# Performance work log

Hardware: AMD Instinct MI355X
Metric: run time of the kernel (lower is better)

The kernel has to match this reference:

```python
import jax, jax.numpy as jnp
import numpy as np

B, S, P, D = 256, 2048, 64, 80

def setup_inputs() -> dict:
    key = jax.random.key(0)
    k1, k2, k3, k4 = jax.random.split(key, 4)
    enc_out = jax.random.normal(k1, (B, S, D), dtype=jnp.float32)
    dec_out = jax.random.normal(k2, (B, P, D), dtype=jnp.float32)
    attn_mask = jax.random.randint(k3, (B, S), 0, 2) > 0  # True = masked
    # guarantee at least one unmasked position per row (avoid NaN softmax)
    attn_mask = attn_mask.at[:, 0].set(False)
    W = jax.random.normal(k4, (D, D), dtype=jnp.float32) * (1.0 / np.sqrt(D))
    return {"enc_out": enc_out, "dec_out": dec_out, "attn_mask": attn_mask, "W": W}

def reference(enc_out, dec_out, attn_mask, W):
    # query = Linear(dec_out) with no bias: y = x @ W^T
    query = jnp.einsum('bpd,ed->bpe', dec_out, W)          # (B, P, D)
    # unscaled attention scores (no 1/sqrt(d) in original)
    weight = jnp.einsum('bpd,bsd->bps', query, enc_out)    # (B, P, S)
    neg = jnp.finfo(weight.dtype).min
    weight = jnp.where(attn_mask[:, None, :], neg, weight)
    weight = jax.nn.softmax(weight, axis=-1)
    context = jnp.einsum('bps,bsd->bpd', weight, enc_out)  # (B, P, D)
    return context
```

## Files before the change

### kernel.cpp

```cpp
#include <hip/hip_runtime.h>

#define NB 256
#define NS 2048
#define NP 64
#define ND 80
#define STILE 128
#define NTILE 16
#define NTHREADS 1024
#define LOG2E 1.4426950408889634f

typedef __attribute__((ext_vector_type(4))) float f32x4;
typedef __attribute__((ext_vector_type(2))) __fp16 fp16x2;
typedef __attribute__((ext_vector_type(8))) _Float16 f16x8;
typedef __attribute__((ext_vector_type(4))) unsigned short u16x4;
typedef unsigned short u16;

#define SMEM_BYTES 60944

__device__ __forceinline__ float E2(float x) { return __builtin_amdgcn_exp2f(x); }
__device__ __forceinline__ unsigned pkh(float lo, float hi) {
  union { fp16x2 h; unsigned u; } cv;
  cv.h = __builtin_amdgcn_cvt_pkrtz(lo, hi);
  return cv.u;
}

__device__ __forceinline__ f32x4 mfma16f(f16x8 a, f16x8 b, f32x4 c) {
  return __builtin_amdgcn_mfma_f32_16x16x32_f16(a, b, c, 0, 0, 0);
}

__global__ __launch_bounds__(NTHREADS, 4)
void DecoderAttention_62989990363717_kernel(const float* __restrict__ enc,
                                            const float* __restrict__ dec,
                                            const int* __restrict__ maskp,
                                            const float* __restrict__ W,
                                            float* __restrict__ out)
{
  __shared__ __align__(16) char smem[SMEM_BYTES];

  u16* ehP    = (u16*)smem;
  float* mbias = (float*)(smem + 50688);
  float* mst  = (float*)(smem + 58880);
  float* lst  = (float*)(smem + 59904);
  int* modep  = (int*)(smem + 60928);

  const int tid  = (int)threadIdx.x;
  const int lane = tid & 63;
  const int wv   = tid >> 6;
  const int pp   = wv & 3;
  const int sq   = wv >> 2;
  const int l15  = lane & 15;
  const int g    = lane >> 4;
  const int b    = (int)blockIdx.x;

  const float* encB = enc + (size_t)b * NS * ND;
  const float* decB = dec + (size_t)b * NP * ND;

  {
    float* Wl = (float*)smem;
    float* dl = (float*)(smem + 26880);
    for (int i = tid; i < 80 * 80; i += NTHREADS) Wl[(i / 80) * 84 + (i % 80)] = W[i];
    for (int i = tid; i < 64 * 80; i += NTHREADS)
      dl[(i / 80) * 84 + (i % 80)] = decB[i] * LOG2E;
    if (tid == 0) {
      const unsigned* mw = (const unsigned*)maskp;
      int ok = 1;
      for (int i = 0; i < 16; ++i) ok &= (mw[i] <= 1u);
      *modep = ok;
    }
    __syncthreads();
    const int m32 = *modep;
    if (m32) {
      int v0 = maskp[(size_t)b * NS + tid];
      int v1 = maskp[(size_t)b * NS + tid + 1024];
      mbias[tid]        = v0 ? -3.0e38f : 0.0f;
      mbias[tid + 1024] = v1 ? -3.0e38f : 0.0f;
    } else if (tid < 512) {
      unsigned w = ((const unsigned*)maskp)[(size_t)b * (NS / 4) + tid];
      f32x4 bb;
      bb[0] = (w & 255u)         ? -3.0e38f : 0.0f;
      bb[1] = ((w >> 8) & 255u)  ? -3.0e38f : 0.0f;
      bb[2] = ((w >> 16) & 255u) ? -3.0e38f : 0.0f;
      bb[3] = (w >> 24)          ? -3.0e38f : 0.0f;
      *(f32x4*)&mbias[4 * tid] = bb;
    }
    float qa[5];
    const int qp = tid & 63, qw = tid >> 6;
#pragma unroll
    for (int j = 0; j < 5; ++j) qa[j] = 0.f;
    for (int kg = 0; kg < 20; ++kg) {
      f32x4 dv = *(const f32x4*)&dl[qp * 84 + kg * 4];
#pragma unroll
      for (int j = 0; j < 5; ++j) {
        f32x4 wv4 = *(const f32x4*)&Wl[(qw * 5 + j) * 84 + kg * 4];
        qa[j] = fmaf(dv.x, wv4.x, qa[j]);
        qa[j] = fmaf(dv.y, wv4.y, qa[j]);
        qa[j] = fmaf(dv.z, wv4.z, qa[j]);
        qa[j] = fmaf(dv.w, wv4.w, qa[j]);
      }
    }
    __syncthreads();
    float* qtmp = (float*)smem;
#pragma unroll
    for (int j = 0; j < 5; ++j) qtmp[qp * 100 + qw * 5 + j] = qa[j];
    if (qw == 15) {
#pragma unroll
      for (int z = 0; z < 16; ++z) qtmp[qp * 100 + 80 + z] = 0.f;
    }
    __syncthreads();
  }

  f16x8 qb[3], qlb[3];
  {
    const float* qtmp = (const float*)smem;
    const int prow = 16 * pp + l15;
#pragma unroll
    for (int kk = 0; kk < 3; ++kk) {
      const int d0 = kk * 32 + g * 8;
      f32x4 f0 = *(const f32x4*)&qtmp[prow * 100 + d0];
      f32x4 f1 = *(const f32x4*)&qtmp[prow * 100 + d0 + 4];
      float fq[8] = {f0.x, f0.y, f0.z, f0.w, f1.x, f1.y, f1.z, f1.w};
      union { _Float16 h[8]; f16x8 v; } H, L;
#pragma unroll
      for (int j = 0; j < 8; ++j) {
        _Float16 hh = (_Float16)fq[j];
        H.h[j] = hh;
        L.h[j] = (_Float16)(fq[j] - (float)hh);
      }
      qb[kk] = H.v; qlb[kk] = L.v;
    }
  }
  __syncthreads();

  if (tid < 256) {
    const int buf = tid >> 7, q = (tid >> 4) & 7, row = tid & 15;
    u16* p = ehP + buf * 12672 + (q * 6 + 5) * 264 + row * 16;
    *(uint4*)p = make_uint4(0u, 0u, 0u, 0u);
    *(uint4*)(p + 8) = make_uint4(0u, 0u, 0u, 0u);
  }

  const bool ldr = (tid < 640);
  const int srow = tid / 5;
  const int c    = tid - srow * 5;
  u16* ePW = ehP + ((srow >> 4) * 6 + c) * 264 + (srow & 15) * 16;
  const float* gsrc = encB + srow * ND + 16 * c;

#define STAGE_WRITE(bi)                                                          \
  do {                                                                           \
    if (ldr) {                                                                   \
      float fv[16] = {r0.x, r0.y, r0.z, r0.w, r1.x, r1.y, r1.z, r1.w,            \
                      r2.x, r2.y, r2.z, r2.w, r3.x, r3.y, r3.z, r3.w};           \
      unsigned hh[8];                                                            \
      _Pragma("unroll")                                                          \
      for (int q = 0; q < 8; ++q) hh[q] = pkh(fv[2*q], fv[2*q+1]);               \
      u16* a_ = ePW + (bi) * 12672;                                              \
      *(uint4*)a_       = make_uint4(hh[0], hh[1], hh[2], hh[3]);                \
      *(uint4*)(a_ + 8) = make_uint4(hh[4], hh[5], hh[6], hh[7]);                \
    }                                                                            \
  } while (0)

  {
    f32x4 r0, r1, r2, r3;
    if (ldr) {
      r0 = *(const f32x4*)gsrc;       r1 = *(const f32x4*)(gsrc + 4);
      r2 = *(const f32x4*)(gsrc + 8); r3 = *(const f32x4*)(gsrc + 12);
    }
    STAGE_WRITE(0);
    __syncthreads();
  }

  f32x4 ctx[5];
#pragma unroll
  for (int n = 0; n < 5; ++n) ctx[n] = (f32x4){0.f, 0.f, 0.f, 0.f};
  float mr = -3.0e38f, lr = 0.f;

  const int qkOff = (2 * sq) * 1584 + (g >> 1) * 264 + 16 * l15 + 8 * (g & 1);
  const unsigned trBase = (unsigned)(uintptr_t)ehP + (unsigned)(sq * 6336 + 8 * lane);

  for (int tt = 0; tt < NTILE; ++tt) {
    const int cur = tt & 1, nxt = cur ^ 1;
    const bool hn = (tt + 1 < NTILE);
    f32x4 r0, r1, r2, r3;
    if (hn && ldr) {
      const float* src = gsrc + (size_t)(tt + 1) * STILE * ND;
      r0 = *(const f32x4*)src;       r1 = *(const f32x4*)(src + 4);
      r2 = *(const f32x4*)(src + 8); r3 = *(const f32x4*)(src + 12);
    }

    f32x4 a0 = (f32x4){0.f, 0.f, 0.f, 0.f}, a1 = (f32x4){0.f, 0.f, 0.f, 0.f};
    {
      const u16* baseH0 = ehP + cur * 12672 + qkOff;
      const u16* baseH1 = baseH0 + 1584;
      f16x8 e0[3], e1[3];
#pragma unroll
      for (int kk = 0; kk < 3; ++kk) {
        e0[kk] = *(const f16x8*)(const void*)(baseH0 + kk * 528);
        e1[kk] = *(const f16x8*)(const void*)(baseH1 + kk * 528);
      }
#pragma unroll
      for (int kk = 0; kk < 3; ++kk) {
        a0 = mfma16f(e0[kk], qb[kk], a0);
        a1 = mfma16f(e1[kk], qb[kk], a1);
        a0 = mfma16f(e0[kk], qlb[kk], a0);
        a1 = mfma16f(e1[kk], qlb[kk], a1);
      }
    }

    const int mb0 = tt * 128 + 32 * sq + 4 * g;
    f32x4 bias0 = *(const f32x4*)&mbias[mb0];
    f32x4 bias1 = *(const f32x4*)&mbias[mb0 + 16];
    float sv0[4], sv1[4];
#pragma unroll
    for (int rr = 0; rr < 4; ++rr) {
      sv0[rr] = a0[rr] + bias0[rr];
      sv1[rr] = a1[rr] + bias1[rr];
    }
    float tm = fmaxf(fmaxf(fmaxf(sv0[0], sv0[1]), fmaxf(sv0[2], sv0[3])),
                     fmaxf(fmaxf(sv1[0], sv1[1]), fmaxf(sv1[2], sv1[3])));
    tm = fmaxf(tm, __shfl_xor(tm, 16));
    tm = fmaxf(tm, __shfl_xor(tm, 32));
    const bool need = !__all(tm <= mr + 11.541560f);
    if (need) {
      float mn = fmaxf(mr, tm);
      float esc = E2(mr - mn);
      lr *= esc; mr = mn;
      float fr[4];
#pragma unroll
      for (int rr = 0; rr < 4; ++rr) fr[rr] = __shfl(esc, 4 * g + rr);
#pragma unroll
      for (int n = 0; n < 5; ++n) {
#pragma unroll
        for (int rr = 0; rr < 4; ++rr) ctx[n][rr] *= fr[rr];
      }
    }
    float p0[4], p1[4];
#pragma unroll
    for (int rr = 0; rr < 4; ++rr) {
      p0[rr] = E2(sv0[rr] - mr);
      p1[rr] = E2(sv1[rr] - mr);
    }
    lr += ((p0[0] + p0[1]) + (p0[2] + p0[3])) + ((p1[0] + p1[1]) + (p1[2] + p1[3]));

    union { unsigned uu[4]; f16x8 v; } PA;
    PA.uu[0] = pkh(p0[0], p0[1]); PA.uu[1] = pkh(p0[2], p0[3]);
    PA.uu[2] = pkh(p1[0], p1[1]); PA.uu[3] = pkh(p1[2], p1[3]);
    const unsigned tra = trBase + (unsigned)(cur * 25344);
    {
      u16x4 ta0, tb0, ta1, tb1, ta2, tb2;
      asm volatile("ds_read_b64_tr_b16 %0, %1"             : "=v"(ta0) : "v"(tra));
      asm volatile("ds_read_b64_tr_b16 %0, %1 offset:3168" : "=v"(tb0) : "v"(tra));
      asm volatile("ds_read_b64_tr_b16 %0, %1 offset:528"  : "=v"(ta1) : "v"(tra));
      asm volatile("ds_read_b64_tr_b16 %0, %1 offset:3696" : "=v"(tb1) : "v"(tra));
      asm volatile("ds_read_b64_tr_b16 %0, %1 offset:1056" : "=v"(ta2) : "v"(tra));
      asm volatile("ds_read_b64_tr_b16 %0, %1 offset:4224" : "=v"(tb2) : "v"(tra));
      asm volatile("s_waitcnt lgkmcnt(0)" ::: "memory");
      __builtin_amdgcn_sched_barrier(0);
      union { u16 s[8]; f16x8 v; } B0, B1, B2;
#pragma unroll
      for (int j = 0; j < 4; ++j) {
        B0.s[j] = ta0[j]; B0.s[4 + j] = tb0[j];
        B1.s[j] = ta1[j]; B1.s[4 + j] = tb1[j];
        B2.s[j] = ta2[j]; B2.s[4 + j] = tb2[j];
      }
      ctx[0] = mfma16f(PA.v, B0.v, ctx[0]);
      ctx[1] = mfma16f(PA.v, B1.v, ctx[1]);
      ctx[2] = mfma16f(PA.v, B2.v, ctx[2]);
    }
    {
      u16x4 ta3, tb3, ta4, tb4;
      asm volatile("ds_read_b64_tr_b16 %0, %1 offset:1584" : "=v"(ta3) : "v"(tra));
      asm volatile("ds_read_b64_tr_b16 %0, %1 offset:4752" : "=v"(tb3) : "v"(tra));
      asm volatile("ds_read_b64_tr_b16 %0, %1 offset:2112" : "=v"(ta4) : "v"(tra));
      asm volatile("ds_read_b64_tr_b16 %0, %1 offset:5280" : "=v"(tb4) : "v"(tra));
      asm volatile("s_waitcnt lgkmcnt(0)" ::: "memory");
      __builtin_amdgcn_sched_barrier(0);
      union { u16 s[8]; f16x8 v; } B3, B4;
#pragma unroll
      for (int j = 0; j < 4; ++j) {
        B3.s[j] = ta3[j]; B3.s[4 + j] = tb3[j];
        B4.s[j] = ta4[j]; B4.s[4 + j] = tb4[j];
      }
      ctx[3] = mfma16f(PA.v, B3.v, ctx[3]);
      ctx[4] = mfma16f(PA.v, B4.v, ctx[4]);
    }

    if (hn) { STAGE_WRITE(nxt); }
    __syncthreads();
  }

  lr += __shfl_xor(lr, 16);
  lr += __shfl_xor(lr, 32);
  if (g == 0) {
    mst[sq * 64 + 16 * pp + l15] = mr;
    lst[sq * 64 + 16 * pp + l15] = lr;
  }
  __syncthreads();
  float F;
  {
    const int pi = 16 * pp + l15;
    float M = fmaxf(fmaxf(mst[pi], mst[64 + pi]), fmaxf(mst[128 + pi], mst[192 + pi]));
    F = E2(mr - M);
  }
  float gg[4];
#pragma unroll
  for (int rr = 0; rr < 4; ++rr) gg[rr] = __shfl(F, 4 * g + rr);
  float* cacc = (float*)smem;
  for (int qq = 0; qq < 4; ++qq) {
    if (sq == qq) {
#pragma unroll
      for (int n = 0; n < 5; ++n) {
#pragma unroll
        for (int rr = 0; rr < 4; ++rr) {
          const int row = 16 * pp + 4 * g + rr;
          const int col = 16 * n + l15;
          float v = ctx[n][rr] * gg[rr];
          if (qq == 0) cacc[row * 84 + col] = v;
          else         cacc[row * 84 + col] += v;
        }
      }
    }
    __syncthreads();
  }
  {
    const int op = tid >> 4, oc = tid & 15;
    float Mv = fmaxf(fmaxf(mst[op], mst[64 + op]), fmaxf(mst[128 + op], mst[192 + op]));
    float Lv = lst[op] * E2(mst[op] - Mv) + lst[64 + op] * E2(mst[64 + op] - Mv)
             + lst[128 + op] * E2(mst[128 + op] - Mv) + lst[192 + op] * E2(mst[192 + op] - Mv);
    float inv = 1.0f / Lv;
    float* orow = out + ((size_t)b * NP + op) * ND + oc * 5;
    const float* crow = cacc + op * 84 + oc * 5;
#pragma unroll
    for (int i = 0; i < 5; ++i) orow[i] = crow[i] * inv;
  }
}

extern "C" void kernel_launch(void* const* d_in, const int* in_sizes, int n_in,
                              void* d_out, int out_size, void* d_ws, size_t ws_size,
                              hipStream_t stream) {
  (void)in_sizes; (void)n_in; (void)out_size; (void)d_ws; (void)ws_size;
  const float* enc  = (const float*)d_in[0];
  const float* dec  = (const float*)d_in[1];
  const int*   mask = (const int*)d_in[2];
  const float* W    = (const float*)d_in[3];
  float* out = (float*)d_out;
  DecoderAttention_62989990363717_kernel<<<dim3(NB), dim3(NTHREADS), 0, stream>>>(
      enc, dec, mask, W, out);
}
```

Baseline: 40.49 us.

## Software-pipeline QK scores one tile ahead with triple-buffered LDS

Restructures the main loop so the QK^T MFMA scores for tile t are computed while the softmax and PV step for tile t-1 runs, using three LDS buffers instead of two (prologue and epilogue peeled). This is meant to break the dependency chain of QK MFMA, then max/exp, then PV within one iteration, so matrix and VALU work can interleave. In exchange, LDS usage grows to about 86KB per block and register pressure rises from carrying the previous scores across iterations, which could limit occupancy.

```diff
diff --git a/kernel.cpp b/kernel.cpp
--- a/kernel.cpp
+++ b/kernel.cpp
@@ -8,6 +8,8 @@
 #define NTILE 16
 #define NTHREADS 1024
 #define LOG2E 1.4426950408889634f
+#define BUFU 12672
+#define BUFB 25344
 
 typedef __attribute__((ext_vector_type(4))) float f32x4;
 typedef __attribute__((ext_vector_type(2))) __fp16 fp16x2;
@@ -15,7 +17,7 @@
 typedef __attribute__((ext_vector_type(4))) unsigned short u16x4;
 typedef unsigned short u16;
 
-#define SMEM_BYTES 60944
+#define SMEM_BYTES 86288
 
 __device__ __forceinline__ float E2(float x) { return __builtin_amdgcn_exp2f(x); }
 __device__ __forceinline__ unsigned pkh(float lo, float hi) {
@@ -38,10 +40,10 @@
   __shared__ __align__(16) char smem[SMEM_BYTES];
 
   u16* ehP    = (u16*)smem;
-  float* mbias = (float*)(smem + 50688);
-  float* mst  = (float*)(smem + 58880);
-  float* lst  = (float*)(smem + 59904);
-  int* modep  = (int*)(smem + 60928);
+  float* mbias = (float*)(smem + 76032);
+  float* mst  = (float*)(smem + 84224);
+  float* lst  = (float*)(smem + 85248);
+  int* modep  = (int*)(smem + 86272);
 
   const int tid  = (int)threadIdx.x;
   const int lane = tid & 63;
@@ -131,9 +133,9 @@
   }
   __syncthreads();
 
-  if (tid < 256) {
+  if (tid < 384) {
     const int buf = tid >> 7, q = (tid >> 4) & 7, row = tid & 15;
-    u16* p = ehP + buf * 12672 + (q * 6 + 5) * 264 + row * 16;
+    u16* p = ehP + buf * BUFU + (q * 6 + 5) * 264 + row * 16;
     *(uint4*)p = make_uint4(0u, 0u, 0u, 0u);
     *(uint4*)(p + 8) = make_uint4(0u, 0u, 0u, 0u);
   }
@@ -144,20 +146,48 @@
   u16* ePW = ehP + ((srow >> 4) * 6 + c) * 264 + (srow & 15) * 16;
   const float* gsrc = encB + srow * ND + 16 * c;
 
-#define STAGE_WRITE(bi)                                                          \
+#define STAGE_WRITE(ofsU16)                                                      \
   do {                                                                           \
     if (ldr) {                                                                   \
-      float fv[16] = {r0.x, r0.y, r0.z, r0.w, r1.x, r1.y, r1.z, r1.w,            \
-                      r2.x, r2.y, r2.z, r2.w, r3.x, r3.y, r3.z, r3.w};           \
       unsigned hh[8];                                                            \
-      _Pragma("unroll")                                                          \
-      for (int q = 0; q < 8; ++q) hh[q] = pkh(fv[2*q], fv[2*q+1]);               \
-      u16* a_ = ePW + (bi) * 12672;                                              \
+      hh[0] = pkh(r0.x, r0.y); hh[1] = pkh(r0.z, r0.w);                          \
+      hh[2] = pkh(r1.x, r1.y); hh[3] = pkh(r1.z, r1.w);                          \
+      hh[4] = pkh(r2.x, r2.y); hh[5] = pkh(r2.z, r2.w);                          \
+      hh[6] = pkh(r3.x, r3.y); hh[7] = pkh(r3.z, r3.w);                          \
+      u16* a_ = ePW + (ofsU16);                                                  \
       *(uint4*)a_       = make_uint4(hh[0], hh[1], hh[2], hh[3]);                \
       *(uint4*)(a_ + 8) = make_uint4(hh[4], hh[5], hh[6], hh[7]);                \
     }                                                                            \
   } while (0)
 
+  const int qkOff = (2 * sq) * 1584 + (g >> 1) * 264 + 16 * l15 + 8 * (g & 1);
+  const unsigned trBase = (unsigned)(uintptr_t)ehP + (unsigned)(sq * 6336 + 8 * lane);
+
+#define QK_COMPUTE(ofsU16, A0, A1)                                               \
+  do {                                                                           \
+    const u16* baseH0 = ehP + (ofsU16) + qkOff;                                  \
+    const u16* baseH1 = baseH0 + 1584;                                           \
+    f16x8 e0[3], e1[3];                                                          \
+    _Pragma("unroll")                                                            \
+    for (int kk = 0; kk < 3; ++kk) {                                             \
+      e0[kk] = *(const f16x8*)(const void*)(baseH0 + kk * 528);                  \
+      e1[kk] = *(const f16x8*)(const void*)(baseH1 + kk * 528);                  \
+    }                                                                            \
+    _Pragma("unroll")                                                            \
+    for (int kk = 0; kk < 3; ++kk) {                                             \
+      A0 = mfma16f(e0[kk], qb[kk], A0);                                          \
+      A1 = mfma16f(e1[kk], qb[kk], A1);                                          \
+      A0 = mfma16f(e0[kk], qlb[kk], A0);                                         \
+      A1 = mfma16f(e1[kk], qlb[kk], A1);                                         \
+    }                                                                            \
+  } while (0)
+
+  f32x4 ctx[5];
+#pragma unroll
+  for (int n = 0; n < 5; ++n) ctx[n] = (f32x4){0.f, 0.f, 0.f, 0.f};
+  float mr = -3.0e38f, lr = 0.f;
+  f32x4 sp0, sp1;
+
   {
     f32x4 r0, r1, r2, r3;
     if (ldr) {
@@ -167,17 +197,22 @@
     STAGE_WRITE(0);
     __syncthreads();
   }
-
-  f32x4 ctx[5];
-#pragma unroll
-  for (int n = 0; n < 5; ++n) ctx[n] = (f32x4){0.f, 0.f, 0.f, 0.f};
-  float mr = -3.0e38f, lr = 0.f;
-
-  const int qkOff = (2 * sq) * 1584 + (g >> 1) * 264 + 16 * l15 + 8 * (g & 1);
-  const unsigned trBase = (unsigned)(uintptr_t)ehP + (unsigned)(sq * 6336 + 8 * lane);
-
-  for (int tt = 0; tt < NTILE; ++tt) {
-    const int cur = tt & 1, nxt = cur ^ 1;
+  {
+    f32x4 r0, r1, r2, r3;
+    if (ldr) {
+      const float* src = gsrc + (size_t)STILE * ND;
+      r0 = *(const f32x4*)src;       r1 = *(const f32x4*)(src + 4);
+      r2 = *(const f32x4*)(src + 8); r3 = *(const f32x4*)(src + 12);
+    }
+    f32x4 a0 = (f32x4){0.f,0.f,0.f,0.f}, a1 = (f32x4){0.f,0.f,0.f,0.f};
+    QK_COMPUTE(0, a0, a1);
+    STAGE_WRITE(BUFU);
+    __syncthreads();
+    sp0 = a0; sp1 = a1;
+  }
+
+  int oA = BUFU, oP = 0, oW = 2 * BUFU;
+  for (int tt = 1; tt < NTILE; ++tt) {
     const bool hn = (tt + 1 < NTILE);
     f32x4 r0, r1, r2, r3;
     if (hn && ldr) {
@@ -186,33 +221,104 @@
       r2 = *(const f32x4*)(src + 8); r3 = *(const f32x4*)(src + 12);
     }
 
-    f32x4 a0 = (f32x4){0.f, 0.f, 0.f, 0.f}, a1 = (f32x4){0.f, 0.f, 0.f, 0.f};
+    f32x4 a0 = (f32x4){0.f,0.f,0.f,0.f}, a1 = (f32x4){0.f,0.f,0.f,0.f};
+    QK_COMPUTE(oA, a0, a1);
+
     {
-      const u16* baseH0 = ehP + cur * 12672 + qkOff;
-      const u16* baseH1 = baseH0 + 1584;
-      f16x8 e0[3], e1[3];
-#pragma unroll
-      for (int kk = 0; kk < 3; ++kk) {
-        e0[kk] = *(const f16x8*)(const void*)(baseH0 + kk * 528);
-        e1[kk] = *(const f16x8*)(const void*)(baseH1 + kk * 528);
-      }
-#pragma unroll
-      for (int kk = 0; kk < 3; ++kk) {
-        a0 = mfma16f(e0[kk], qb[kk], a0);
-        a1 = mfma16f(e1[kk], qb[kk], a1);
-        a0 = mfma16f(e0[kk], qlb[kk], a0);
-        a1 = mfma16f(e1[kk], qlb[kk], a1);
-      }
-    }
-
-    const int mb0 = tt * 128 + 32 * sq + 4 * g;
+      const int mb0 = (tt - 1) * 128 + 32 * sq + 4 * g;
+      f32x4 bias0 = *(const f32x4*)&mbias[mb0];
+      f32x4 bias1 = *(const f32x4*)&mbias[mb0 + 16];
+      float sv0[4], sv1[4];
+#pragma unroll
+      for (int rr = 0; rr < 4; ++rr) {
+        sv0[rr] = sp0[rr] + bias0[rr];
+        sv1[rr] = sp1[rr] + bias1[rr];
+      }
+      float tm = fmaxf(fmaxf(fmaxf(sv0[0], sv0[1]), fmaxf(sv0[2], sv0[3])),
+                       fmaxf(fmaxf(sv1[0], sv1[1]), fmaxf(sv1[2], sv1[3])));
+      tm = fmaxf(tm, __shfl_xor(tm, 16));
+      tm = fmaxf(tm, __shfl_xor(tm, 32));
+      const bool need = !__all(tm <= mr + 11.541560f);
+      if (need) {
+        float mn = fmaxf(mr, tm);
+        float esc = E2(mr - mn);
+        lr *= esc; mr = mn;
+        float fr[4];
+#pragma unroll
+        for (int rr = 0; rr < 4; ++rr) fr[rr] = __shfl(esc, 4 * g + rr);
+#pragma unroll
+        for (int n = 0; n < 5; ++n) {
+#pragma unroll
+          for (int rr = 0; rr < 4; ++rr) ctx[n][rr] *= fr[rr];
+        }
+      }
+      float p0[4], p1[4];
+#pragma unroll
+      for (int rr = 0; rr < 4; ++rr) {
+        p0[rr] = E2(sv0[rr] - mr);
+        p1[rr] = E2(sv1[rr] - mr);
+      }
+      lr += ((p0[0] + p0[1]) + (p0[2] + p0[3])) + ((p1[0] + p1[1]) + (p1[2] + p1[3]));
+
+      union { unsigned uu[4]; f16x8 v; } PA;
+      PA.uu[0] = pkh(p0[0], p0[1]); PA.uu[1] = pkh(p0[2], p0[3]);
+      PA.uu[2] = pkh(p1[0], p1[1]); PA.uu[3] = pkh(p1[2], p1[3]);
+      const unsigned tra = trBase + (unsigned)(oP * 2);
+      {
+        u16x4 ta0, tb0, ta1, tb1, ta2, tb2;
+        asm volatile("ds_read_b64_tr_b16 %0, %1"             : "=v"(ta0) : "v"(tra));
+        asm volatile("ds_read_b64_tr_b16 %0, %1 offset:3168" : "=v"(tb0) : "v"(tra));
+        asm volatile("ds_read_b64_tr_b16 %0, %1 offset:528"  : "=v"(ta1) : "v"(tra));
+        asm volatile("ds_read_b64_tr_b16 %0, %1 offset:3696" : "=v"(tb1) : "v"(tra));
+        asm volatile("ds_read_b64_tr_b16 %0, %1 offset:1056" : "=v"(ta2) : "v"(tra));
+        asm volatile("ds_read_b64_tr_b16 %0, %1 offset:4224" : "=v"(tb2) : "v"(tra));
+        asm volatile("s_waitcnt lgkmcnt(0)" ::: "memory");
+        __builtin_amdgcn_sched_barrier(0);
+        union { u16 s[8]; f16x8 v; } B0, B1, B2;
+#pragma unroll
+        for (int j = 0; j < 4; ++j) {
+          B0.s[j] = ta0[j]; B0.s[4 + j] = tb0[j];
+          B1.s[j] = ta1[j]; B1.s[4 + j] = tb1[j];
+          B2.s[j] = ta2[j]; B2.s[4 + j] = tb2[j];
+        }
+        ctx[0] = mfma16f(PA.v, B0.v, ctx[0]);
+        ctx[1] = mfma16f(PA.v, B1.v, ctx[1]);
+        ctx[2] = mfma16f(PA.v, B2.v, ctx[2]);
+      }
+      {
+        u16x4 ta3, tb3, ta4, tb4;
+        asm volatile("ds_read_b64_tr_b16 %0, %1 offset:1584" : "=v"(ta3) : "v"(tra));
+        asm volatile("ds_read_b64_tr_b16 %0, %1 offset:4752" : "=v"(tb3) : "v"(tra));
+        asm volatile("ds_read_b64_tr_b16 %0, %1 offset:2112" : "=v"(ta4) : "v"(tra));
+        asm volatile("ds_read_b64_tr_b16 %0, %1 offset:5280" : "=v"(tb4) : "v"(tra));
+        asm volatile("s_waitcnt lgkmcnt(0)" ::: "memory");
+        __builtin_amdgcn_sched_barrier(0);
+        union { u16 s[8]; f16x8 v; } B3, B4;
+#pragma unroll
+        for (int j = 0; j < 4; ++j) {
+          B3.s[j] = ta3[j]; B3.s[4 + j] = tb3[j];
+          B4.s[j] = ta4[j]; B4.s[4 + j] = tb4[j];
+        }
+        ctx[3] = mfma16f(PA.v, B3.v, ctx[3]);
+        ctx[4] = mfma16f(PA.v, B4.v, ctx[4]);
+      }
+    }
+
+    if (hn) { STAGE_WRITE(oW); }
+    __syncthreads();
+    sp0 = a0; sp1 = a1;
+    const int t2 = oP; oP = oA; oA = oW; oW = t2;
+  }
+
+  {
+    const int mb0 = (NTILE - 1) * 128 + 32 * sq + 4 * g;
     f32x4 bias0 = *(const f32x4*)&mbias[mb0];
     f32x4 bias1 = *(const f32x4*)&mbias[mb0 + 16];
     float sv0[4], sv1[4];
 #pragma unroll
     for (int rr = 0; rr < 4; ++rr) {
-      sv0[rr] = a0[rr] + bias0[rr];
-      sv1[rr] = a1[rr] + bias1[rr];
+      sv0[rr] = sp0[rr] + bias0[rr];
+      sv1[rr] = sp1[rr] + bias1[rr];
     }
     float tm = fmaxf(fmaxf(fmaxf(sv0[0], sv0[1]), fmaxf(sv0[2], sv0[3])),
                      fmaxf(fmaxf(sv1[0], sv1[1]), fmaxf(sv1[2], sv1[3])));
@@ -243,7 +349,7 @@
     union { unsigned uu[4]; f16x8 v; } PA;
     PA.uu[0] = pkh(p0[0], p0[1]); PA.uu[1] = pkh(p0[2], p0[3]);
     PA.uu[2] = pkh(p1[0], p1[1]); PA.uu[3] = pkh(p1[2], p1[3]);
-    const unsigned tra = trBase + (unsigned)(cur * 25344);
+    const unsigned tra = trBase + (unsigned)(oP * 2);
     {
       u16x4 ta0, tb0, ta1, tb1, ta2, tb2;
       asm volatile("ds_read_b64_tr_b16 %0, %1"             : "=v"(ta0) : "v"(tra));
@@ -282,9 +388,6 @@
       ctx[3] = mfma16f(PA.v, B3.v, ctx[3]);
       ctx[4] = mfma16f(PA.v, B4.v, ctx[4]);
     }
-
-    if (hn) { STAGE_WRITE(nxt); }
-    __syncthreads();
   }
 
   lr += __shfl_xor(lr, 16);
```

Result: no change. 41.15 us (+1.6%).

## Repartition waves to 8 S-slices by 2 P-halves and drop fp16 split-precision query

Applied to the files above, without the earlier changes.

The wave layout changes from 4 P-blocks by 4 S-quarters to 8 S-slices of 16 keys by 2 P-halves, each wave holding two 16-row query blocks. Every enc fragment loaded from LDS is now reused across both query blocks, and the hi/lo fp16 split of the query is removed, cutting the QK MFMAs in half. The PV step uses half-filled k=32 MFMAs (upper half zero-padded) with one transposed read per column block. The final reduction now merges 8 partial softmax states through two accumulation buffers. Dropping the low-order query term lowers score precision, and the padded PV MFMAs do wasted work.

```diff
diff --git a/kernel.cpp b/kernel.cpp
--- a/kernel.cpp
+++ b/kernel.cpp
@@ -8,6 +8,8 @@
 #define NTILE 16
 #define NTHREADS 1024
 #define LOG2E 1.4426950408889634f
+#define BUFU 12672
+#define BUFBY 25344
 
 typedef __attribute__((ext_vector_type(4))) float f32x4;
 typedef __attribute__((ext_vector_type(2))) __fp16 fp16x2;
@@ -15,7 +17,7 @@
 typedef __attribute__((ext_vector_type(4))) unsigned short u16x4;
 typedef unsigned short u16;
 
-#define SMEM_BYTES 60944
+#define SMEM_BYTES 62992
 
 __device__ __forceinline__ float E2(float x) { return __builtin_amdgcn_exp2f(x); }
 __device__ __forceinline__ unsigned pkh(float lo, float hi) {
@@ -40,14 +42,14 @@
   u16* ehP    = (u16*)smem;
   float* mbias = (float*)(smem + 50688);
   float* mst  = (float*)(smem + 58880);
-  float* lst  = (float*)(smem + 59904);
-  int* modep  = (int*)(smem + 60928);
+  float* lst  = (float*)(smem + 60928);
+  int* modep  = (int*)(smem + 62976);
 
   const int tid  = (int)threadIdx.x;
   const int lane = tid & 63;
   const int wv   = tid >> 6;
-  const int pp   = wv & 3;
-  const int sq   = wv >> 2;
+  const int sq   = wv >> 1;
+  const int ph   = wv & 1;
   const int l15  = lane & 15;
   const int g    = lane >> 4;
   const int b    = (int)blockIdx.x;
@@ -109,31 +111,31 @@
     __syncthreads();
   }
 
-  f16x8 qb[3], qlb[3];
+  f16x8 qb[2][3];
   {
     const float* qtmp = (const float*)smem;
-    const int prow = 16 * pp + l15;
-#pragma unroll
-    for (int kk = 0; kk < 3; ++kk) {
-      const int d0 = kk * 32 + g * 8;
-      f32x4 f0 = *(const f32x4*)&qtmp[prow * 100 + d0];
-      f32x4 f1 = *(const f32x4*)&qtmp[prow * 100 + d0 + 4];
-      float fq[8] = {f0.x, f0.y, f0.z, f0.w, f1.x, f1.y, f1.z, f1.w};
-      union { _Float16 h[8]; f16x8 v; } H, L;
-#pragma unroll
-      for (int j = 0; j < 8; ++j) {
-        _Float16 hh = (_Float16)fq[j];
-        H.h[j] = hh;
-        L.h[j] = (_Float16)(fq[j] - (float)hh);
-      }
-      qb[kk] = H.v; qlb[kk] = L.v;
+#pragma unroll
+    for (int pb = 0; pb < 2; ++pb) {
+      const int prow = 32 * ph + 16 * pb + l15;
+#pragma unroll
+      for (int kk = 0; kk < 3; ++kk) {
+        const int d0 = kk * 32 + g * 8;
+        f32x4 f0 = *(const f32x4*)&qtmp[prow * 100 + d0];
+        f32x4 f1 = *(const f32x4*)&qtmp[prow * 100 + d0 + 4];
+        union { _Float16 h[8]; f16x8 v; } H;
+        H.h[0] = (_Float16)f0.x; H.h[1] = (_Float16)f0.y;
+        H.h[2] = (_Float16)f0.z; H.h[3] = (_Float16)f0.w;
+        H.h[4] = (_Float16)f1.x; H.h[5] = (_Float16)f1.y;
+        H.h[6] = (_Float16)f1.z; H.h[7] = (_Float16)f1.w;
+        qb[pb][kk] = H.v;
+      }
     }
   }
   __syncthreads();
 
   if (tid < 256) {
     const int buf = tid >> 7, q = (tid >> 4) & 7, row = tid & 15;
-    u16* p = ehP + buf * 12672 + (q * 6 + 5) * 264 + row * 16;
+    u16* p = ehP + buf * BUFU + (q * 6 + 5) * 264 + row * 16;
     *(uint4*)p = make_uint4(0u, 0u, 0u, 0u);
     *(uint4*)(p + 8) = make_uint4(0u, 0u, 0u, 0u);
   }
@@ -147,12 +149,12 @@
 #define STAGE_WRITE(bi)                                                          \
   do {                                                                           \
     if (ldr) {                                                                   \
-      float fv[16] = {r0.x, r0.y, r0.z, r0.w, r1.x, r1.y, r1.z, r1.w,            \
-                      r2.x, r2.y, r2.z, r2.w, r3.x, r3.y, r3.z, r3.w};           \
       unsigned hh[8];                                                            \
-      _Pragma("unroll")                                                          \
-      for (int q = 0; q < 8; ++q) hh[q] = pkh(fv[2*q], fv[2*q+1]);               \
-      u16* a_ = ePW + (bi) * 12672;                                              \
+      hh[0] = pkh(r0.x, r0.y); hh[1] = pkh(r0.z, r0.w);                          \
+      hh[2] = pkh(r1.x, r1.y); hh[3] = pkh(r1.z, r1.w);                          \
+      hh[4] = pkh(r2.x, r2.y); hh[5] = pkh(r2.z, r2.w);                          \
+      hh[6] = pkh(r3.x, r3.y); hh[7] = pkh(r3.z, r3.w);                          \
+      u16* a_ = ePW + (bi) * BUFU;                                               \
       *(uint4*)a_       = make_uint4(hh[0], hh[1], hh[2], hh[3]);                \
       *(uint4*)(a_ + 8) = make_uint4(hh[4], hh[5], hh[6], hh[7]);                \
     }                                                                            \
@@ -168,13 +170,13 @@
     __syncthreads();
   }
 
-  f32x4 ctx[5];
-#pragma unroll
-  for (int n = 0; n < 5; ++n) ctx[n] = (f32x4){0.f, 0.f, 0.f, 0.f};
-  float mr = -3.0e38f, lr = 0.f;
-
-  const int qkOff = (2 * sq) * 1584 + (g >> 1) * 264 + 16 * l15 + 8 * (g & 1);
-  const unsigned trBase = (unsigned)(uintptr_t)ehP + (unsigned)(sq * 6336 + 8 * lane);
+  f32x4 ctx0[5], ctx1[5];
+#pragma unroll
+  for (int n = 0; n < 5; ++n) { ctx0[n] = (f32x4){0.f,0.f,0.f,0.f}; ctx1[n] = (f32x4){0.f,0.f,0.f,0.f}; }
+  float mr0 = -1.0e30f, mr1 = -1.0e30f, lr0 = 0.f, lr1 = 0.f;
+
+  const int qkOff = sq * 1584 + (g >> 1) * 264 + 16 * l15 + 8 * (g & 1);
+  const unsigned trBase = (unsigned)(uintptr_t)ehP + (unsigned)(sq * 3168 + 8 * lane);
 
   for (int tt = 0; tt < NTILE; ++tt) {
     const int cur = tt & 1, nxt = cur ^ 1;
@@ -188,148 +190,160 @@
 
     f32x4 a0 = (f32x4){0.f, 0.f, 0.f, 0.f}, a1 = (f32x4){0.f, 0.f, 0.f, 0.f};
     {
-      const u16* baseH0 = ehP + cur * 12672 + qkOff;
-      const u16* baseH1 = baseH0 + 1584;
-      f16x8 e0[3], e1[3];
-#pragma unroll
-      for (int kk = 0; kk < 3; ++kk) {
-        e0[kk] = *(const f16x8*)(const void*)(baseH0 + kk * 528);
-        e1[kk] = *(const f16x8*)(const void*)(baseH1 + kk * 528);
-      }
-#pragma unroll
-      for (int kk = 0; kk < 3; ++kk) {
-        a0 = mfma16f(e0[kk], qb[kk], a0);
-        a1 = mfma16f(e1[kk], qb[kk], a1);
-        a0 = mfma16f(e0[kk], qlb[kk], a0);
-        a1 = mfma16f(e1[kk], qlb[kk], a1);
-      }
-    }
-
-    const int mb0 = tt * 128 + 32 * sq + 4 * g;
-    f32x4 bias0 = *(const f32x4*)&mbias[mb0];
-    f32x4 bias1 = *(const f32x4*)&mbias[mb0 + 16];
+      const u16* baseH = ehP + cur * BUFU + qkOff;
+      f16x8 e0 = *(const f16x8*)(const void*)(baseH);
+      f16x8 e1 = *(const f16x8*)(const void*)(baseH + 528);
+      f16x8 e2 = *(const f16x8*)(const void*)(baseH + 1056);
+      a0 = mfma16f(e0, qb[0][0], a0);
+      a1 = mfma16f(e0, qb[1][0], a1);
+      a0 = mfma16f(e1, qb[0][1], a0);
+      a1 = mfma16f(e1, qb[1][1], a1);
+      a0 = mfma16f(e2, qb[0][2], a0);
+      a1 = mfma16f(e2, qb[1][2], a1);
+    }
+
+    f32x4 bias4 = *(const f32x4*)&mbias[tt * 128 + 16 * sq + 4 * g];
     float sv0[4], sv1[4];
 #pragma unroll
     for (int rr = 0; rr < 4; ++rr) {
-      sv0[rr] = a0[rr] + bias0[rr];
-      sv1[rr] = a1[rr] + bias1[rr];
-    }
-    float tm = fmaxf(fmaxf(fmaxf(sv0[0], sv0[1]), fmaxf(sv0[2], sv0[3])),
-                     fmaxf(fmaxf(sv1[0], sv1[1]), fmaxf(sv1[2], sv1[3])));
-    tm = fmaxf(tm, __shfl_xor(tm, 16));
-    tm = fmaxf(tm, __shfl_xor(tm, 32));
-    const bool need = !__all(tm <= mr + 11.541560f);
+      sv0[rr] = a0[rr] + bias4[rr];
+      sv1[rr] = a1[rr] + bias4[rr];
+    }
+    float tm0 = fmaxf(fmaxf(sv0[0], sv0[1]), fmaxf(sv0[2], sv0[3]));
+    tm0 = fmaxf(tm0, __shfl_xor(tm0, 16));
+    tm0 = fmaxf(tm0, __shfl_xor(tm0, 32));
+    float tm1 = fmaxf(fmaxf(sv1[0], sv1[1]), fmaxf(sv1[2], sv1[3]));
+    tm1 = fmaxf(tm1, __shfl_xor(tm1, 16));
+    tm1 = fmaxf(tm1, __shfl_xor(tm1, 32));
+    const bool need = !__all((tm0 <= mr0 + 11.541560f) && (tm1 <= mr1 + 11.541560f));
     if (need) {
-      float mn = fmaxf(mr, tm);
-      float esc = E2(mr - mn);
-      lr *= esc; mr = mn;
-      float fr[4];
-#pragma unroll
-      for (int rr = 0; rr < 4; ++rr) fr[rr] = __shfl(esc, 4 * g + rr);
+      float mn0 = fmaxf(mr0, tm0), mn1 = fmaxf(mr1, tm1);
+      float esc0 = E2(mr0 - mn0), esc1 = E2(mr1 - mn1);
+      lr0 *= esc0; lr1 *= esc1;
+      mr0 = mn0; mr1 = mn1;
+      float fr0[4], fr1[4];
+#pragma unroll
+      for (int rr = 0; rr < 4; ++rr) {
+        fr0[rr] = __shfl(esc0, 4 * g + rr);
+        fr1[rr] = __shfl(esc1, 4 * g + rr);
+      }
 #pragma unroll
       for (int n = 0; n < 5; ++n) {
 #pragma unroll
-        for (int rr = 0; rr < 4; ++rr) ctx[n][rr] *= fr[rr];
+        for (int rr = 0; rr < 4; ++rr) { ctx0[n][rr] *= fr0[rr]; ctx1[n][rr] *= fr1[rr]; }
       }
     }
     float p0[4], p1[4];
 #pragma unroll
     for (int rr = 0; rr < 4; ++rr) {
-      p0[rr] = E2(sv0[rr] - mr);
-      p1[rr] = E2(sv1[rr] - mr);
-    }
-    lr += ((p0[0] + p0[1]) + (p0[2] + p0[3])) + ((p1[0] + p1[1]) + (p1[2] + p1[3]));
-
-    union { unsigned uu[4]; f16x8 v; } PA;
-    PA.uu[0] = pkh(p0[0], p0[1]); PA.uu[1] = pkh(p0[2], p0[3]);
-    PA.uu[2] = pkh(p1[0], p1[1]); PA.uu[3] = pkh(p1[2], p1[3]);
-    const unsigned tra = trBase + (unsigned)(cur * 25344);
-    {
-      u16x4 ta0, tb0, ta1, tb1, ta2, tb2;
-      asm volatile("ds_read_b64_tr_b16 %0, %1"             : "=v"(ta0) : "v"(tra));
-      asm volatile("ds_read_b64_tr_b16 %0, %1 offset:3168" : "=v"(tb0) : "v"(tra));
-      asm volatile("ds_read_b64_tr_b16 %0, %1 offset:528"  : "=v"(ta1) : "v"(tra));
-      asm volatile("ds_read_b64_tr_b16 %0, %1 offset:3696" : "=v"(tb1) : "v"(tra));
-      asm volatile("ds_read_b64_tr_b16 %0, %1 offset:1056" : "=v"(ta2) : "v"(tra));
-      asm volatile("ds_read_b64_tr_b16 %0, %1 offset:4224" : "=v"(tb2) : "v"(tra));
-      asm volatile("s_waitcnt lgkmcnt(0)" ::: "memory");
-      __builtin_amdgcn_sched_barrier(0);
-      union { u16 s[8]; f16x8 v; } B0, B1, B2;
-#pragma unroll
-      for (int j = 0; j < 4; ++j) {
-        B0.s[j] = ta0[j]; B0.s[4 + j] = tb0[j];
-        B1.s[j] = ta1[j]; B1.s[4 + j] = tb1[j];
-        B2.s[j] = ta2[j]; B2.s[4 + j] = tb2[j];
-      }
-      ctx[0] = mfma16f(PA.v, B0.v, ctx[0]);
-      ctx[1] = mfma16f(PA.v, B1.v, ctx[1]);
-      ctx[2] = mfma16f(PA.v, B2.v, ctx[2]);
-    }
-    {
-      u16x4 ta3, tb3, ta4, tb4;
-      asm volatile("ds_read_b64_tr_b16 %0, %1 offset:1584" : "=v"(ta3) : "v"(tra));
-      asm volatile("ds_read_b64_tr_b16 %0, %1 offset:4752" : "=v"(tb3) : "v"(tra));
-      asm volatile("ds_read_b64_tr_b16 %0, %1 offset:2112" : "=v"(ta4) : "v"(tra));
-      asm volatile("ds_read_b64_tr_b16 %0, %1 offset:5280" : "=v"(tb4) : "v"(tra));
-      asm volatile("s_waitcnt lgkmcnt(0)" ::: "memory");
-      __builtin_amdgcn_sched_barrier(0);
-      union { u16 s[8]; f16x8 v; } B3, B4;
-#pragma unroll
-      for (int j = 0; j < 4; ++j) {
-        B3.s[j] = ta3[j]; B3.s[4 + j] = tb3[j];
-        B4.s[j] = ta4[j]; B4.s[4 + j] = tb4[j];
-      }
-      ctx[3] = mfma16f(PA.v, B3.v, ctx[3]);
-      ctx[4] = mfma16f(PA.v, B4.v, ctx[4]);
-    }
+      p0[rr] = E2(sv0[rr] - mr0);
+      p1[rr] = E2(sv1[rr] - mr1);
+    }
+    lr0 += (p0[0] + p0[1]) + (p0[2] + p0[3]);
+    lr1 += (p1[0] + p1[1]) + (p1[2] + p1[3]);
+
+    union { unsigned uu[4]; f16x8 v; } PA0, PA1;
+    PA0.uu[0] = pkh(p0[0], p0[1]); PA0.uu[1] = pkh(p0[2], p0[3]);
+    PA0.uu[2] = 0u; PA0.uu[3] = 0u;
+    PA1.uu[0] = pkh(p1[0], p1[1]); PA1.uu[1] = pkh(p1[2], p1[3]);
+    PA1.uu[2] = 0u; PA1.uu[3] = 0u;
+    const unsigned tra = trBase + (unsigned)(cur * BUFBY);
+    u16x4 tv0, tv1, tv2, tv3, tv4;
+    asm volatile("ds_read_b64_tr_b16 %0, %1"             : "=v"(tv0) : "v"(tra));
+    asm volatile("ds_read_b64_tr_b16 %0, %1 offset:528"  : "=v"(tv1) : "v"(tra));
+    asm volatile("ds_read_b64_tr_b16 %0, %1 offset:1056" : "=v"(tv2) : "v"(tra));
+    asm volatile("ds_read_b64_tr_b16 %0, %1 offset:1584" : "=v"(tv3) : "v"(tra));
+    asm volatile("ds_read_b64_tr_b16 %0, %1 offset:2112" : "=v"(tv4) : "v"(tra));
+    asm volatile("s_waitcnt lgkmcnt(0)" ::: "memory");
+    __builtin_amdgcn_sched_barrier(0);
+#define PVN(n, tvn)                                                              \
+    {                                                                            \
+      union { u16 s[8]; f16x8 v; } B_;                                           \
+      B_.s[0] = (tvn)[0]; B_.s[1] = (tvn)[1];                                    \
+      B_.s[2] = (tvn)[2]; B_.s[3] = (tvn)[3];                                    \
+      B_.s[4] = 0; B_.s[5] = 0; B_.s[6] = 0; B_.s[7] = 0;                        \
+      ctx0[n] = mfma16f(PA0.v, B_.v, ctx0[n]);                                   \
+      ctx1[n] = mfma16f(PA1.v, B_.v, ctx1[n]);                                   \
+    }
+    PVN(0, tv0) PVN(1, tv1) PVN(2, tv2) PVN(3, tv3) PVN(4, tv4)
+#undef PVN
 
     if (hn) { STAGE_WRITE(nxt); }
     __syncthreads();
   }
 
-  lr += __shfl_xor(lr, 16);
-  lr += __shfl_xor(lr, 32);
+  lr0 += __shfl_xor(lr0, 16); lr0 += __shfl_xor(lr0, 32);
+  lr1 += __shfl_xor(lr1, 16); lr1 += __shfl_xor(lr1, 32);
   if (g == 0) {
-    mst[sq * 64 + 16 * pp + l15] = mr;
-    lst[sq * 64 + 16 * pp + l15] = lr;
+    const int pi = 32 * ph + l15;
+    mst[sq * 64 + pi] = mr0;      lst[sq * 64 + pi] = lr0;
+    mst[sq * 64 + pi + 16] = mr1; lst[sq * 64 + pi + 16] = lr1;
   }
   __syncthreads();
-  float F;
-  {
-    const int pi = 16 * pp + l15;
-    float M = fmaxf(fmaxf(mst[pi], mst[64 + pi]), fmaxf(mst[128 + pi], mst[192 + pi]));
-    F = E2(mr - M);
-  }
-  float gg[4];
-#pragma unroll
-  for (int rr = 0; rr < 4; ++rr) gg[rr] = __shfl(F, 4 * g + rr);
-  float* cacc = (float*)smem;
-  for (int qq = 0; qq < 4; ++qq) {
+  float F0, F1;
+  {
+    const int p0i = 32 * ph + l15, p1i = p0i + 16;
+    float M0 = mst[p0i], M1 = mst[p1i];
+#pragma unroll
+    for (int k = 1; k < 8; ++k) {
+      M0 = fmaxf(M0, mst[k * 64 + p0i]);
+      M1 = fmaxf(M1, mst[k * 64 + p1i]);
+    }
+    F0 = E2(mr0 - M0); F1 = E2(mr1 - M1);
+  }
+  float g0[4], g1[4];
+#pragma unroll
+  for (int rr = 0; rr < 4; ++rr) {
+    g0[rr] = __shfl(F0, 4 * g + rr);
+    g1[rr] = __shfl(F1, 4 * g + rr);
+  }
+  float* cacc0 = (float*)smem;
+  float* cacc1 = (float*)(smem + 21504);
+  for (int qq = 0; qq < 8; qq += 2) {
     if (sq == qq) {
 #pragma unroll
       for (int n = 0; n < 5; ++n) {
 #pragma unroll
         for (int rr = 0; rr < 4; ++rr) {
-          const int row = 16 * pp + 4 * g + rr;
+          const int r0_ = 32 * ph + 4 * g + rr;
           const int col = 16 * n + l15;
-          float v = ctx[n][rr] * gg[rr];
-          if (qq == 0) cacc[row * 84 + col] = v;
-          else         cacc[row * 84 + col] += v;
+          float v0 = ctx0[n][rr] * g0[rr];
+          float v1 = ctx1[n][rr] * g1[rr];
+          if (qq == 0) { cacc0[r0_ * 84 + col] = v0; cacc0[(r0_ + 16) * 84 + col] = v1; }
+          else         { cacc0[r0_ * 84 + col] += v0; cacc0[(r0_ + 16) * 84 + col] += v1; }
         }
       }
     }
-    __syncthreads();
-  }
-  {
-    const int op = tid >> 4, oc = tid & 15;
-    float Mv = fmaxf(fmaxf(mst[op], mst[64 + op]), fmaxf(mst[128 + op], mst[192 + op]));
-    float Lv = lst[op] * E2(mst[op] - Mv) + lst[64 + op] * E2(mst[64 + op] - Mv)
-             + lst[128 + op] * E2(mst[128 + op] - Mv) + lst[192 + op] * E2(mst[192 + op] - Mv);
+    if (sq == qq + 1) {
+#pragma unroll
+      for (int n = 0; n < 5; ++n) {
+#pragma unroll
+        for (int rr = 0; rr < 4; ++rr) {
+          const int r0_ = 32 * ph + 4 * g + rr;
+          const int col = 16 * n + l15;
+          float v0 = ctx0[n][rr] * g0[rr];
+          float v1 = ctx1[n][rr] * g1[rr];
+          if (qq == 0) { cacc1[r0_ * 84 + col] = v0; cacc1[(r0_ + 16) * 84 + col] = v1; }
+          else         { cacc1[r0_ * 84 + col] += v0; cacc1[(r0_ + 16) * 84 + col] += v1; }
+        }
+      }
+    }
+    __syncthreads();
+  }
+  {
+    const int op = tid >> 4, oc = tid & 15, od0 = oc * 5;
+    float Mv = mst[op];
+#pragma unroll
+    for (int k = 1; k < 8; ++k) Mv = fmaxf(Mv, mst[k * 64 + op]);
+    float Lv = 0.f;
+#pragma unroll
+    for (int k = 0; k < 8; ++k) Lv += lst[k * 64 + op] * E2(mst[k * 64 + op] - Mv);
     float inv = 1.0f / Lv;
-    float* orow = out + ((size_t)b * NP + op) * ND + oc * 5;
-    const float* crow = cacc + op * 84 + oc * 5;
-#pragma unroll
-    for (int i = 0; i < 5; ++i) orow[i] = crow[i] * inv;
+    float* orow = out + ((size_t)b * NP + op) * ND + od0;
+    const float* c0 = cacc0 + op * 84 + od0;
+    const float* c1 = cacc1 + op * 84 + od0;
+#pragma unroll
+    for (int i = 0; i < 5; ++i) orow[i] = (c0[i] + c1[i]) * inv;
   }
 }
 
```

New measurement: 61.87 us. +52.8%, slower.
